# Kernel tuning notes

Measured on AMD Instinct MI355X. Metric: run time of the kernel, lower is better.

Reference implementation:

```python
import jax, jax.numpy as jnp
import numpy as np

K = 2  # top-k experts per token


def setup_inputs() -> dict:
    key = jax.random.key(0)
    kx, kw = jax.random.split(key)
    N, D, E = 16384, 4096, 64
    x = jax.random.normal(kx, (N, D), dtype=jnp.float32)
    # nn.Linear(input_dim, num_experts, bias=False) weight: [num_experts, input_dim]
    W = jax.random.normal(kw, (E, D), dtype=jnp.float32) * (1.0 / np.sqrt(D))
    return {"x": x, "W": W}


def reference(x, W):
    # logits = x @ W^T : [N, E]
    logits = jnp.einsum('nd,ed->ne', x, W)
    top_k_logits, top_k_indices = jax.lax.top_k(logits, K)  # [N, K]
    top_k_weights = jax.nn.softmax(top_k_logits, axis=-1)   # softmax over the k selected
    N = logits.shape[0]
    rows = jnp.arange(N)[:, None]  # [N, 1] broadcast against [N, K]
    full_weights = jnp.zeros_like(logits).at[rows, top_k_indices].set(top_k_weights)
    return full_weights, top_k_indices
```

## Files before the change

kernel.cpp:

```cpp
#include <hip/hip_runtime.h>
#include <math.h>

#define N_TOK 16384
#define DDIM  4096
#define NEXP  64
#define TM    32
#define KHALF 2048
#define LSTR  68
#define TAU   1e-3f

typedef __attribute__((ext_vector_type(8))) short bf16x8;
typedef __attribute__((ext_vector_type(4))) float f32x4;

__device__ __forceinline__ void split8(f32x4 v0, f32x4 v1, bf16x8& hi, bf16x8& lo) {
    float f[8];
    *(f32x4*)&f[0] = v0;  *(f32x4*)&f[4] = v1;
    #pragma unroll
    for (int i = 0; i < 8; ++i) {
        unsigned u  = __float_as_uint(f[i]);
        unsigned uh = u & 0xFFFF0000u;
        float    rf = f[i] - __uint_as_float(uh);
        hi[i] = (short)(u >> 16);
        lo[i] = (short)(__float_as_uint(rf) >> 16);
    }
}

__global__ __launch_bounds__(256) void topk_gate_kernel(
    const float* __restrict__ x, const float* __restrict__ W,
    float* __restrict__ out)
{
    __shared__ float  Lgh[2][TM][LSTR];
    __shared__ int    top_i[TM * 2];
    __shared__ float  top_w[TM * 2];
    __shared__ int    nflag;
    __shared__ int    flist[TM];
    __shared__ double red[256];
    __shared__ double lgd[NEXP];
    __shared__ int    rbi[2];
    __shared__ float  rbw[2];

    const int tid  = threadIdx.x;
    const int lane = tid & 63;
    const int w    = tid >> 6;
    const int tg   = w & 1;
    const int half = w >> 1;
    const int block_tok = blockIdx.x * TM;

    const int r16  = lane & 15;
    const int koct = lane >> 4;

    const float* xp = x + (size_t)(block_tok + tg * 16 + r16) * DDIM
                        + half * KHALF + koct * 8;
    const float* wp0 = W + (size_t)r16 * DDIM + half * KHALF + koct * 8;

    f32x4 acc[4];
    #pragma unroll
    for (int t = 0; t < 4; ++t) acc[t] = (f32x4){0.f, 0.f, 0.f, 0.f};

    #pragma unroll 2
    for (int kb = 0; kb < KHALF; kb += 32) {
        f32x4 a0 = *(const f32x4*)(xp + kb);
        f32x4 a1 = *(const f32x4*)(xp + kb + 4);
        bf16x8 ah, al;
        split8(a0, a1, ah, al);
        #pragma unroll
        for (int t = 0; t < 4; ++t) {
            const float* wp = wp0 + (size_t)t * 16 * DDIM + kb;
            f32x4 b0 = *(const f32x4*)(wp);
            f32x4 b1 = *(const f32x4*)(wp + 4);
            bf16x8 bh, bl;
            split8(b0, b1, bh, bl);
            acc[t] = __builtin_amdgcn_mfma_f32_16x16x32_bf16(ah, bh, acc[t], 0, 0, 0);
            acc[t] = __builtin_amdgcn_mfma_f32_16x16x32_bf16(ah, bl, acc[t], 0, 0, 0);
            acc[t] = __builtin_amdgcn_mfma_f32_16x16x32_bf16(al, bh, acc[t], 0, 0, 0);
        }
    }

    #pragma unroll
    for (int t = 0; t < 4; ++t)
        #pragma unroll
        for (int r = 0; r < 4; ++r)
            Lgh[half][tg * 16 + koct * 4 + r][t * 16 + r16] = acc[t][r];
    if (tid == 0) nflag = 0;
    __syncthreads();

    if (tid < TM) {
        float m1 = -INFINITY, m2 = -INFINITY, m3 = -INFINITY;
        int i1 = 0, i2 = 0;
        for (int e = 0; e < NEXP; ++e) {
            float v = Lgh[0][tid][e] + Lgh[1][tid][e];
            if (v > m1)      { m3 = m2; m2 = m1; i2 = i1; m1 = v; i1 = e; }
            else if (v > m2) { m3 = m2; m2 = v; i2 = e; }
            else if (v > m3) { m3 = v; }
        }
        float d  = expf(m2 - m1);
        float rn = 1.0f / (1.0f + d);
        top_i[tid * 2 + 0] = i1;  top_i[tid * 2 + 1] = i2;
        top_w[tid * 2 + 0] = rn;  top_w[tid * 2 + 1] = d * rn;
        float2* oi = (float2*)(out + (size_t)N_TOK * NEXP);
        oi[block_tok + tid] = make_float2((float)i1, (float)i2);
        if ((m1 - m2 < TAU) || (m2 - m3 < TAU)) {
            int p = atomicAdd(&nflag, 1);
            flist[p] = tid;
        }
    }
    __syncthreads();

    float4* ow = (float4*)(out + (size_t)block_tok * NEXP);
    #pragma unroll
    for (int jj = 0; jj < 2; ++jj) {
        int flat = tid + jj * 256;
        int tok  = flat >> 4;
        int e4   = (flat & 15) * 4;
        int a1 = top_i[tok * 2], a2 = top_i[tok * 2 + 1];
        float v1 = top_w[tok * 2], v2 = top_w[tok * 2 + 1];
        float4 v; float* vp = (float*)&v;
        #pragma unroll
        for (int q = 0; q < 4; ++q) {
            int e = e4 + q;
            vp[q] = (e == a1) ? v1 : ((e == a2) ? v2 : 0.0f);
        }
        ow[flat] = v;
    }
    __syncthreads();

    const int fn = nflag;
    for (int f = 0; f < fn; ++f) {
        const int tok = block_tok + flist[f];
        const int e = tid & 63, q = tid >> 6;
        const float* wr = W + (size_t)e * DDIM + q * (DDIM / 4);
        const float* xr = x + (size_t)tok * DDIM + q * (DDIM / 4);
        double p = 0.0;
        for (int k = 0; k < DDIM / 4; k += 4) {
            float4 wv = *(const float4*)(wr + k);
            float4 xv = *(const float4*)(xr + k);
            p += (double)xv.x * (double)wv.x;
            p += (double)xv.y * (double)wv.y;
            p += (double)xv.z * (double)wv.z;
            p += (double)xv.w * (double)wv.w;
        }
        red[tid] = p;
        __syncthreads();
        if (tid < 64) lgd[tid] = red[tid] + red[tid + 64] + red[tid + 128] + red[tid + 192];
        __syncthreads();

        if (tid == 0) {
            double m1 = -INFINITY, m2 = -INFINITY;
            int i1 = 0, i2 = 0;
            for (int ee = 0; ee < NEXP; ++ee) {
                double v = lgd[ee];
                if (v > m1)      { m2 = m1; i2 = i1; m1 = v; i1 = ee; }
                else if (v > m2) { m2 = v; i2 = ee; }
            }
            double d  = exp(m2 - m1);
            double rn = 1.0 / (1.0 + d);
            rbi[0] = i1; rbi[1] = i2;
            rbw[0] = (float)rn; rbw[1] = (float)(d * rn);
            float2* oi = (float2*)(out + (size_t)N_TOK * NEXP);
            oi[tok] = make_float2((float)i1, (float)i2);
        }
        __syncthreads();

        if (tid < 16) {
            float4 v = make_float4(0.f, 0.f, 0.f, 0.f);
            float* vp = (float*)&v;
            #pragma unroll
            for (int qq = 0; qq < 4; ++qq) {
                int ee = tid * 4 + qq;
                if (ee == rbi[0]) vp[qq] = rbw[0];
                else if (ee == rbi[1]) vp[qq] = rbw[1];
            }
            ((float4*)(out + (size_t)tok * NEXP))[tid] = v;
        }
        __syncthreads();
    }
}

extern "C" void kernel_launch(void* const* d_in, const int* in_sizes, int n_in,
                              void* d_out, int out_size, void* d_ws, size_t ws_size,
                              hipStream_t stream) {
    const float* x = (const float*)d_in[0];
    const float* W = (const float*)d_in[1];
    float* out = (float*)d_out;
    (void)in_sizes; (void)n_in; (void)d_ws; (void)ws_size; (void)out_size;

    hipLaunchKernelGGL(topk_gate_kernel, dim3(N_TOK / TM), dim3(256), 0, stream,
                       x, W, out);
}
```

Measured before the change: 582.5 us.

## Split K dimension eight ways with 1024-thread blocks and LDS reduction

The K dimension is split into eight slices instead of two, and each block grows from 256 to 1024 threads, so each wave covers a quarter as much K. Partial logits from the eight slices are summed in shared memory before the top-2 selection, and the fp64 fallback path is spread over 512 threads. The aim is more waves per CU, since the old grid gave only about eight waves per CU, to hide global load latency. In exchange, shared memory per block grows to about 70KB, which limits blocks per CU. The aggressive launch bound may also squeeze registers enough to cause spills.

```diff
diff --git a/kernel.cpp b/kernel.cpp
--- a/kernel.cpp
+++ b/kernel.cpp
@@ -5,7 +5,8 @@
 #define DDIM  4096
 #define NEXP  64
 #define TM    32
-#define KHALF 2048
+#define NSL   8
+#define KSL   (DDIM / NSL)
 #define LSTR  68
 #define TAU   1e-3f
 
@@ -25,16 +26,16 @@
     }
 }
 
-__global__ __launch_bounds__(256) void topk_gate_kernel(
+__global__ __launch_bounds__(1024, 8) void topk_gate_kernel(
     const float* __restrict__ x, const float* __restrict__ W,
     float* __restrict__ out)
 {
-    __shared__ float  Lgh[2][TM][LSTR];
+    __shared__ float  Lgh[NSL][TM][LSTR];
     __shared__ int    top_i[TM * 2];
     __shared__ float  top_w[TM * 2];
     __shared__ int    nflag;
     __shared__ int    flist[TM];
-    __shared__ double red[256];
+    __shared__ double red[512];
     __shared__ double lgd[NEXP];
     __shared__ int    rbi[2];
     __shared__ float  rbw[2];
@@ -43,22 +44,22 @@
     const int lane = tid & 63;
     const int w    = tid >> 6;
     const int tg   = w & 1;
-    const int half = w >> 1;
+    const int ks   = w >> 1;
     const int block_tok = blockIdx.x * TM;
 
     const int r16  = lane & 15;
     const int koct = lane >> 4;
 
     const float* xp = x + (size_t)(block_tok + tg * 16 + r16) * DDIM
-                        + half * KHALF + koct * 8;
-    const float* wp0 = W + (size_t)r16 * DDIM + half * KHALF + koct * 8;
+                        + ks * KSL + koct * 8;
+    const float* wp0 = W + (size_t)r16 * DDIM + ks * KSL + koct * 8;
 
     f32x4 acc[4];
     #pragma unroll
     for (int t = 0; t < 4; ++t) acc[t] = (f32x4){0.f, 0.f, 0.f, 0.f};
 
     #pragma unroll 2
-    for (int kb = 0; kb < KHALF; kb += 32) {
+    for (int kb = 0; kb < KSL; kb += 32) {
         f32x4 a0 = *(const f32x4*)(xp + kb);
         f32x4 a1 = *(const f32x4*)(xp + kb + 4);
         bf16x8 ah, al;
@@ -80,15 +81,28 @@
     for (int t = 0; t < 4; ++t)
         #pragma unroll
         for (int r = 0; r < 4; ++r)
-            Lgh[half][tg * 16 + koct * 4 + r][t * 16 + r16] = acc[t][r];
+            Lgh[ks][tg * 16 + koct * 4 + r][t * 16 + r16] = acc[t][r];
     if (tid == 0) nflag = 0;
+    __syncthreads();
+
+    if (tid < 512) {
+        const int tok = tid >> 4;
+        const int e4  = (tid & 15) * 4;
+        float4 s = *(const float4*)&Lgh[0][tok][e4];
+        #pragma unroll
+        for (int h = 1; h < NSL; ++h) {
+            float4 v = *(const float4*)&Lgh[h][tok][e4];
+            s.x += v.x; s.y += v.y; s.z += v.z; s.w += v.w;
+        }
+        *(float4*)&Lgh[0][tok][e4] = s;
+    }
     __syncthreads();
 
     if (tid < TM) {
         float m1 = -INFINITY, m2 = -INFINITY, m3 = -INFINITY;
         int i1 = 0, i2 = 0;
         for (int e = 0; e < NEXP; ++e) {
-            float v = Lgh[0][tid][e] + Lgh[1][tid][e];
+            float v = Lgh[0][tid][e];
             if (v > m1)      { m3 = m2; m2 = m1; i2 = i1; m1 = v; i1 = e; }
             else if (v > m2) { m3 = m2; m2 = v; i2 = e; }
             else if (v > m3) { m3 = v; }
@@ -106,12 +120,10 @@
     }
     __syncthreads();
 
-    float4* ow = (float4*)(out + (size_t)block_tok * NEXP);
-    #pragma unroll
-    for (int jj = 0; jj < 2; ++jj) {
-        int flat = tid + jj * 256;
-        int tok  = flat >> 4;
-        int e4   = (flat & 15) * 4;
+    if (tid < 512) {
+        float4* ow = (float4*)(out + (size_t)block_tok * NEXP);
+        const int tok = tid >> 4;
+        const int e4  = (tid & 15) * 4;
         int a1 = top_i[tok * 2], a2 = top_i[tok * 2 + 1];
         float v1 = top_w[tok * 2], v2 = top_w[tok * 2 + 1];
         float4 v; float* vp = (float*)&v;
@@ -120,28 +132,35 @@
             int e = e4 + q;
             vp[q] = (e == a1) ? v1 : ((e == a2) ? v2 : 0.0f);
         }
-        ow[flat] = v;
+        ow[tid] = v;
     }
     __syncthreads();
 
     const int fn = nflag;
     for (int f = 0; f < fn; ++f) {
         const int tok = block_tok + flist[f];
-        const int e = tid & 63, q = tid >> 6;
-        const float* wr = W + (size_t)e * DDIM + q * (DDIM / 4);
-        const float* xr = x + (size_t)tok * DDIM + q * (DDIM / 4);
-        double p = 0.0;
-        for (int k = 0; k < DDIM / 4; k += 4) {
-            float4 wv = *(const float4*)(wr + k);
-            float4 xv = *(const float4*)(xr + k);
-            p += (double)xv.x * (double)wv.x;
-            p += (double)xv.y * (double)wv.y;
-            p += (double)xv.z * (double)wv.z;
-            p += (double)xv.w * (double)wv.w;
-        }
-        red[tid] = p;
-        __syncthreads();
-        if (tid < 64) lgd[tid] = red[tid] + red[tid + 64] + red[tid + 128] + red[tid + 192];
+        if (tid < 512) {
+            const int e = tid & 63, q = tid >> 6;
+            const float* wr = W + (size_t)e * DDIM + q * (DDIM / 8);
+            const float* xr = x + (size_t)tok * DDIM + q * (DDIM / 8);
+            double p = 0.0;
+            for (int k = 0; k < DDIM / 8; k += 4) {
+                float4 wv = *(const float4*)(wr + k);
+                float4 xv = *(const float4*)(xr + k);
+                p += (double)xv.x * (double)wv.x;
+                p += (double)xv.y * (double)wv.y;
+                p += (double)xv.z * (double)wv.z;
+                p += (double)xv.w * (double)wv.w;
+            }
+            red[tid] = p;
+        }
+        __syncthreads();
+        if (tid < 64) {
+            double s = 0.0;
+            #pragma unroll
+            for (int j = 0; j < 8; ++j) s += red[tid + 64 * j];
+            lgd[tid] = s;
+        }
         __syncthreads();
 
         if (tid == 0) {
@@ -184,6 +203,6 @@
     float* out = (float*)d_out;
     (void)in_sizes; (void)n_in; (void)d_ws; (void)ws_size; (void)out_size;
 
-    hipLaunchKernelGGL(topk_gate_kernel, dim3(N_TOK / TM), dim3(256), 0, stream,
+    hipLaunchKernelGGL(topk_gate_kernel, dim3(N_TOK / TM), dim3(1024), 0, stream,
                        x, W, out);
 }
```

Result: no change. 575.7 us (-1.2%).

## Stage x and W tiles through swizzled LDS with double-buffered async loads

Applied to the files above, without the earlier changes.

Replaces direct per-lane global loads with global_load_lds async copies into a double-buffered, XOR-swizzled shared-memory tile (BK=128), so that loading the next K-step overlaps with the MFMA work on the current one. The tile grows to 64 tokens per 512-thread block, so each W tile staged in LDS is reused across more tokens, and the two K-halves are summed through LDS. The fallback fp64 recompute is split across 8 waves. The kernel uses 128KB of shared memory with launch_bounds(512,2), which may cap occupancy, and there are half as many blocks.

```diff
diff --git a/kernel.cpp b/kernel.cpp
--- a/kernel.cpp
+++ b/kernel.cpp
@@ -4,10 +4,13 @@
 #define N_TOK 16384
 #define DDIM  4096
 #define NEXP  64
-#define TM    32
-#define KHALF 2048
+#define TM    64
+#define BK    128
+#define NSTEP (DDIM / BK)
 #define LSTR  68
 #define TAU   1e-3f
+
+static_assert(NSTEP % 2 == 0, "pipeline assumes even step count");
 
 typedef __attribute__((ext_vector_type(8))) short bf16x8;
 typedef __attribute__((ext_vector_type(4))) float f32x4;
@@ -25,16 +28,22 @@
     }
 }
 
-__global__ __launch_bounds__(256) void topk_gate_kernel(
+__device__ __forceinline__ void gl2lds16(const void* g, void* l) {
+    __builtin_amdgcn_global_load_lds(
+        (const __attribute__((address_space(1))) unsigned int*)g,
+        (__attribute__((address_space(3))) unsigned int*)l,
+        16, 0, 0);
+}
+
+__global__ __launch_bounds__(512, 2) void topk_gate_kernel(
     const float* __restrict__ x, const float* __restrict__ W,
     float* __restrict__ out)
 {
-    __shared__ float  Lgh[2][TM][LSTR];
+    __shared__ __align__(16) char sraw[2 * 65536];
     __shared__ int    top_i[TM * 2];
     __shared__ float  top_w[TM * 2];
     __shared__ int    nflag;
     __shared__ int    flist[TM];
-    __shared__ double red[256];
     __shared__ double lgd[NEXP];
     __shared__ int    rbi[2];
     __shared__ float  rbw[2];
@@ -42,53 +51,114 @@
     const int tid  = threadIdx.x;
     const int lane = tid & 63;
     const int w    = tid >> 6;
-    const int tg   = w & 1;
-    const int half = w >> 1;
+    const int tt   = w & 3;
+    const int h    = w >> 2;
     const int block_tok = blockIdx.x * TM;
 
     const int r16  = lane & 15;
     const int koct = lane >> 4;
 
-    const float* xp = x + (size_t)(block_tok + tg * 16 + r16) * DDIM
-                        + half * KHALF + koct * 8;
-    const float* wp0 = W + (size_t)r16 * DDIM + half * KHALF + koct * 8;
+    const int l31 = lane & 31;
+    const int qbase = w * 4;
+    const char *xs0, *xs1, *xs2, *xs3, *ws0, *ws1, *ws2, *ws3;
+    {
+        int r0 = (qbase + 0) * 2 + (lane >> 5);
+        int r1 = (qbase + 1) * 2 + (lane >> 5);
+        int r2 = (qbase + 2) * 2 + (lane >> 5);
+        int r3 = (qbase + 3) * 2 + (lane >> 5);
+        int s0 = (l31 * 16) ^ ((r0 & 7) << 4);
+        int s1 = (l31 * 16) ^ ((r1 & 7) << 4);
+        int s2 = (l31 * 16) ^ ((r2 & 7) << 4);
+        int s3 = (l31 * 16) ^ ((r3 & 7) << 4);
+        xs0 = (const char*)x + (size_t)(block_tok + r0) * (DDIM * 4) + s0;
+        xs1 = (const char*)x + (size_t)(block_tok + r1) * (DDIM * 4) + s1;
+        xs2 = (const char*)x + (size_t)(block_tok + r2) * (DDIM * 4) + s2;
+        xs3 = (const char*)x + (size_t)(block_tok + r3) * (DDIM * 4) + s3;
+        ws0 = (const char*)W + (size_t)r0 * (DDIM * 4) + s0;
+        ws1 = (const char*)W + (size_t)r1 * (DDIM * 4) + s1;
+        ws2 = (const char*)W + (size_t)r2 * (DDIM * 4) + s2;
+        ws3 = (const char*)W + (size_t)r3 * (DDIM * 4) + s3;
+    }
+
+#define STAGE(B, ST) do {                                                   \
+    size_t _o = (size_t)(ST) * 512;                                         \
+    char*  _d = sraw + (B) * 65536 + qbase * 1024;                          \
+    gl2lds16(xs0 + _o, _d);          gl2lds16(ws0 + _o, _d + 32768);        \
+    gl2lds16(xs1 + _o, _d + 1024);   gl2lds16(ws1 + _o, _d + 33792);        \
+    gl2lds16(xs2 + _o, _d + 2048);   gl2lds16(ws2 + _o, _d + 34816);        \
+    gl2lds16(xs3 + _o, _d + 3072);   gl2lds16(ws3 + _o, _d + 35840);        \
+} while (0)
+
+    const int Q  = (r16 & 7) << 4;
+    const int pa = (koct * 32) ^ Q;
+    const int pb = (koct * 32 + 16) ^ Q;
 
     f32x4 acc[4];
     #pragma unroll
     for (int t = 0; t < 4; ++t) acc[t] = (f32x4){0.f, 0.f, 0.f, 0.f};
 
-    #pragma unroll 2
-    for (int kb = 0; kb < KHALF; kb += 32) {
-        f32x4 a0 = *(const f32x4*)(xp + kb);
-        f32x4 a1 = *(const f32x4*)(xp + kb + 4);
-        bf16x8 ah, al;
-        split8(a0, a1, ah, al);
-        #pragma unroll
-        for (int t = 0; t < 4; ++t) {
-            const float* wp = wp0 + (size_t)t * 16 * DDIM + kb;
-            f32x4 b0 = *(const f32x4*)(wp);
-            f32x4 b1 = *(const f32x4*)(wp + 4);
-            bf16x8 bh, bl;
-            split8(b0, b1, bh, bl);
-            acc[t] = __builtin_amdgcn_mfma_f32_16x16x32_bf16(ah, bh, acc[t], 0, 0, 0);
-            acc[t] = __builtin_amdgcn_mfma_f32_16x16x32_bf16(ah, bl, acc[t], 0, 0, 0);
-            acc[t] = __builtin_amdgcn_mfma_f32_16x16x32_bf16(al, bh, acc[t], 0, 0, 0);
-        }
-    }
-
+#define COMPUTE(B) do {                                                     \
+    const char* _xb = sraw + (B) * 65536 + (tt * 16 + r16) * 512;           \
+    const char* _wb = sraw + (B) * 65536 + 32768 + r16 * 512;               \
+    _Pragma("unroll")                                                       \
+    for (int ss = 0; ss < 2; ++ss) {                                        \
+        const int sofs = (2 * h + ss) * 128;                                \
+        f32x4 a0 = *(const f32x4*)(_xb + sofs + pa);                        \
+        f32x4 a1 = *(const f32x4*)(_xb + sofs + pb);                        \
+        bf16x8 ah, al;  split8(a0, a1, ah, al);                             \
+        _Pragma("unroll")                                                   \
+        for (int t = 0; t < 4; ++t) {                                       \
+            const char* _wt = _wb + t * 8192;                               \
+            f32x4 b0 = *(const f32x4*)(_wt + sofs + pa);                    \
+            f32x4 b1 = *(const f32x4*)(_wt + sofs + pb);                    \
+            bf16x8 bh, bl;  split8(b0, b1, bh, bl);                         \
+            acc[t] = __builtin_amdgcn_mfma_f32_16x16x32_bf16(ah, bh, acc[t], 0, 0, 0); \
+            acc[t] = __builtin_amdgcn_mfma_f32_16x16x32_bf16(ah, bl, acc[t], 0, 0, 0); \
+            acc[t] = __builtin_amdgcn_mfma_f32_16x16x32_bf16(al, bh, acc[t], 0, 0, 0); \
+        }                                                                   \
+    }                                                                       \
+} while (0)
+
+    STAGE(0, 0);
+    __syncthreads();
+    #pragma unroll 1
+    for (int st = 0; st < NSTEP; st += 2) {
+        if (st + 1 < NSTEP) STAGE(1, st + 1);
+        COMPUTE(0);
+        __syncthreads();
+        if (st + 2 < NSTEP) STAGE(0, st + 2);
+        COMPUTE(1);
+        __syncthreads();
+    }
+
+    float* Lg = (float*)sraw;
     #pragma unroll
     for (int t = 0; t < 4; ++t)
         #pragma unroll
         for (int r = 0; r < 4; ++r)
-            Lgh[half][tg * 16 + koct * 4 + r][t * 16 + r16] = acc[t][r];
+            Lg[(h * 64 + tt * 16 + koct * 4 + r) * LSTR + t * 16 + r16] = acc[t][r];
     if (tid == 0) nflag = 0;
+    __syncthreads();
+
+    {
+        const int tok = tid >> 3;
+        const int e8  = (tid & 7) * 8;
+        float4 s0 = *(float4*)&Lg[tok * LSTR + e8];
+        float4 s1 = *(float4*)&Lg[tok * LSTR + e8 + 4];
+        float4 u0 = *(float4*)&Lg[(64 + tok) * LSTR + e8];
+        float4 u1 = *(float4*)&Lg[(64 + tok) * LSTR + e8 + 4];
+        s0.x += u0.x; s0.y += u0.y; s0.z += u0.z; s0.w += u0.w;
+        s1.x += u1.x; s1.y += u1.y; s1.z += u1.z; s1.w += u1.w;
+        *(float4*)&Lg[tok * LSTR + e8]     = s0;
+        *(float4*)&Lg[tok * LSTR + e8 + 4] = s1;
+    }
     __syncthreads();
 
     if (tid < TM) {
         float m1 = -INFINITY, m2 = -INFINITY, m3 = -INFINITY;
         int i1 = 0, i2 = 0;
         for (int e = 0; e < NEXP; ++e) {
-            float v = Lgh[0][tid][e] + Lgh[1][tid][e];
+            float v = Lg[tid * LSTR + e];
             if (v > m1)      { m3 = m2; m2 = m1; i2 = i1; m1 = v; i1 = e; }
             else if (v > m2) { m3 = m2; m2 = v; i2 = e; }
             else if (v > m3) { m3 = v; }
@@ -106,42 +176,52 @@
     }
     __syncthreads();
 
-    float4* ow = (float4*)(out + (size_t)block_tok * NEXP);
-    #pragma unroll
-    for (int jj = 0; jj < 2; ++jj) {
-        int flat = tid + jj * 256;
-        int tok  = flat >> 4;
-        int e4   = (flat & 15) * 4;
-        int a1 = top_i[tok * 2], a2 = top_i[tok * 2 + 1];
-        float v1 = top_w[tok * 2], v2 = top_w[tok * 2 + 1];
-        float4 v; float* vp = (float*)&v;
+    {
+        float4* ow = (float4*)(out + (size_t)block_tok * NEXP);
         #pragma unroll
-        for (int q = 0; q < 4; ++q) {
-            int e = e4 + q;
-            vp[q] = (e == a1) ? v1 : ((e == a2) ? v2 : 0.0f);
-        }
-        ow[flat] = v;
-    }
-    __syncthreads();
-
+        for (int jj = 0; jj < 2; ++jj) {
+            int flat = tid + jj * 512;
+            int tok  = flat >> 4;
+            int e4   = (flat & 15) * 4;
+            int a1 = top_i[tok * 2], a2 = top_i[tok * 2 + 1];
+            float v1 = top_w[tok * 2], v2 = top_w[tok * 2 + 1];
+            float4 v; float* vp = (float*)&v;
+            #pragma unroll
+            for (int q = 0; q < 4; ++q) {
+                int e = e4 + q;
+                vp[q] = (e == a1) ? v1 : ((e == a2) ? v2 : 0.0f);
+            }
+            ow[flat] = v;
+        }
+    }
+    __syncthreads();
+
+    double* red = (double*)(sraw + 65536);
     const int fn = nflag;
     for (int f = 0; f < fn; ++f) {
         const int tok = block_tok + flist[f];
-        const int e = tid & 63, q = tid >> 6;
-        const float* wr = W + (size_t)e * DDIM + q * (DDIM / 4);
-        const float* xr = x + (size_t)tok * DDIM + q * (DDIM / 4);
-        double p = 0.0;
-        for (int k = 0; k < DDIM / 4; k += 4) {
-            float4 wv = *(const float4*)(wr + k);
-            float4 xv = *(const float4*)(xr + k);
-            p += (double)xv.x * (double)wv.x;
-            p += (double)xv.y * (double)wv.y;
-            p += (double)xv.z * (double)wv.z;
-            p += (double)xv.w * (double)wv.w;
-        }
-        red[tid] = p;
-        __syncthreads();
-        if (tid < 64) lgd[tid] = red[tid] + red[tid + 64] + red[tid + 128] + red[tid + 192];
+        {
+            const int e = tid & 63, q = tid >> 6;
+            const float* wr = W + (size_t)e * DDIM + q * (DDIM / 8);
+            const float* xr = x + (size_t)tok * DDIM + q * (DDIM / 8);
+            double p = 0.0;
+            for (int k = 0; k < DDIM / 8; k += 4) {
+                float4 wv = *(const float4*)(wr + k);
+                float4 xv = *(const float4*)(xr + k);
+                p += (double)xv.x * (double)wv.x;
+                p += (double)xv.y * (double)wv.y;
+                p += (double)xv.z * (double)wv.z;
+                p += (double)xv.w * (double)wv.w;
+            }
+            red[tid] = p;
+        }
+        __syncthreads();
+        if (tid < 64) {
+            double s = 0.0;
+            #pragma unroll
+            for (int j = 0; j < 8; ++j) s += red[tid + 64 * j];
+            lgd[tid] = s;
+        }
         __syncthreads();
 
         if (tid == 0) {
@@ -174,6 +254,8 @@
         }
         __syncthreads();
     }
+#undef STAGE
+#undef COMPUTE
 }
 
 extern "C" void kernel_launch(void* const* d_in, const int* in_sizes, int n_in,
@@ -184,6 +266,6 @@
     float* out = (float*)d_out;
     (void)in_sizes; (void)n_in; (void)d_ws; (void)ws_size; (void)out_size;
 
-    hipLaunchKernelGGL(topk_gate_kernel, dim3(N_TOK / TM), dim3(256), 0, stream,
+    hipLaunchKernelGGL(topk_gate_kernel, dim3(N_TOK / TM), dim3(512), 0, stream,
                        x, W, out);
 }
```

New measurement: 549.5 us. 5.7% less time.
